# Optimization experiments

Measured on AMD Instinct MI355X. Metric: run time of the kernel, lower is better.

Reference implementation:

```python
import jax, jax.numpy as jnp
import numpy as np

EPS = 1e-8


def setup_inputs() -> dict:
    key = jax.random.key(0)
    k1, k2, k3, k4 = jax.random.split(key, 4)
    b, cin, cout, H, W, ksz = 8, 512, 512, 64, 64, 3
    return {
        "x": jax.random.normal(k1, (b, cin, H, W), dtype=jnp.float32),
        "style": jax.random.normal(k2, (b, cin), dtype=jnp.float32),
        "noise": jax.random.normal(k3, (b, 1, H, W), dtype=jnp.float32),
        "weight": jax.random.normal(k4, (cout, cin, ksz, ksz), dtype=jnp.float32),
        "bias": jnp.zeros((1, cout, 1, 1), dtype=jnp.float32),
        "noise_strength": jnp.zeros((), dtype=jnp.float32),
    }


def reference(x, style, noise, weight, bias, noise_strength):
    cout, cin, k, _ = weight.shape
    b, _, H, W = x.shape
    scale = (1.0 / (cin * k * k)) ** 0.5

    # weight scaled and normalized by per-filter inf-norm
    w = weight * scale / jnp.max(jnp.abs(weight), axis=(1, 2, 3), keepdims=True)
    # style normalized by per-sample inf-norm
    s = style / jnp.max(jnp.abs(style), axis=1, keepdims=True)

    # modulate: (b, cout, cin, k, k)
    w = w[None] * s[:, None, :, None, None]
    # demodulate
    demod = jnp.sqrt(jnp.sum(w * w, axis=(2, 3, 4)) + EPS)  # (b, cout)
    w = w / demod[:, :, None, None, None]

    # grouped conv: one group per sample (note: input is scaled again, as in source)
    xr = (x * scale).reshape(1, b * cin, H, W)
    wr = w.reshape(b * cout, cin, k, k)
    out = jax.lax.conv_general_dilated(
        xr, wr, window_strides=(1, 1), padding=((1, 1), (1, 1)),
        dimension_numbers=("NCHW", "OIHW", "NCHW"), feature_group_count=b)
    out = out.reshape(b, cout, H, W) + bias
    out = out + noise * noise_strength
    return out
```

## Files before the change

kernel.cpp:

```cpp
#include <hip/hip_runtime.h>


#define EPSV   1e-8f
#define SCALEV 0.014731391274719738f

typedef __attribute__((ext_vector_type(8))) short short8;
typedef __attribute__((ext_vector_type(4))) float floatx4;

__device__ __forceinline__ void gload_lds16(const void* g, void* l) {
    __builtin_amdgcn_global_load_lds(
        (const __attribute__((address_space(1))) void*)g,
        (__attribute__((address_space(3))) void*)l, 16, 0, 0);
}

__device__ __forceinline__ unsigned short f2bf(float f) {
    unsigned u = __float_as_uint(f);
    unsigned r = (u + 0x7fffu + ((u >> 16) & 1u)) >> 16;
    return (unsigned short)r;
}

__global__ __launch_bounds__(256) void zero_ws(uint4* __restrict__ p, int n4) {
    uint4 z = {0u, 0u, 0u, 0u};
    int stride = gridDim.x * 256;
    for (int i = blockIdx.x * 256 + threadIdx.x; i < n4; i += stride) p[i] = z;
}

__global__ __launch_bounds__(512) void prep_style(
    const float* __restrict__ style, float* __restrict__ tbuf)
{
    const int b = blockIdx.x, t = threadIdx.x;
    float v = style[b * 512 + t];
    __shared__ float red[512];
    red[t] = fabsf(v);
    __syncthreads();
    for (int s = 256; s > 0; s >>= 1) {
        if (t < s) red[t] = fmaxf(red[t], red[t + s]);
        __syncthreads();
    }
    tbuf[b * 512 + t] = v / red[0];
}

__global__ __launch_bounds__(256) void prep_w(
    const float* __restrict__ weight, float* __restrict__ wsqn,
    unsigned short* __restrict__ Aw)
{
    const int co = blockIdx.x, t = threadIdx.x;
    const float* wp = weight + (size_t)co * 4608;
    float m = 0.f;
    for (int i = t; i < 4608; i += 256) m = fmaxf(m, fabsf(wp[i]));
    __shared__ float red[256];
    red[t] = m;
    __syncthreads();
    for (int s = 128; s > 0; s >>= 1) {
        if (t < s) red[t] = fmaxf(red[t], red[t + s]);
        __syncthreads();
    }
    const float inv = 1.f / red[0];
    for (int ci = t; ci < 512; ci += 256) {
        float s = 0.f;
        #pragma unroll
        for (int k = 0; k < 9; ++k) {
            float v = wp[ci * 9 + k] * inv;
            s = fmaf(v, v, s);
            Aw[(size_t)(co * 9 + k) * 512 + ci] = f2bf(v);
        }
        wsqn[co * 512 + ci] = s;
    }
}

__global__ __launch_bounds__(256) void prep_x(
    const float* __restrict__ x, const float* __restrict__ tbuf,
    unsigned short* __restrict__ xbp)
{
    const int cic = blockIdx.x;
    const int h   = blockIdx.y;
    const int b   = blockIdx.z;
    const int tid = threadIdx.x;
    __shared__ float tr[64][33];

    const int cl = tid >> 3;
    const int w0 = (tid & 7) << 3;
    const int ci = cic * 32 + cl;
    const float tv = tbuf[b * 512 + ci];
    const float* xp = x + (((size_t)(b * 512 + ci)) << 12) + (h << 6) + w0;
    float4 u = *(const float4*)xp;
    float4 v = *(const float4*)(xp + 4);
    tr[w0 + 0][cl] = u.x * tv; tr[w0 + 1][cl] = u.y * tv;
    tr[w0 + 2][cl] = u.z * tv; tr[w0 + 3][cl] = u.w * tv;
    tr[w0 + 4][cl] = v.x * tv; tr[w0 + 5][cl] = v.y * tv;
    tr[w0 + 6][cl] = v.z * tv; tr[w0 + 7][cl] = v.w * tv;
    __syncthreads();

    const int w  = tid >> 2;
    const int c8 = (tid & 3) << 3;
    unsigned short o[8] __attribute__((aligned(16)));
    #pragma unroll
    for (int j = 0; j < 8; ++j) o[j] = f2bf(tr[w][c8 + j]);
    size_t dst = ((size_t)((b * 66 + h + 1) * 66) + (w + 1)) * 512 + cic * 32 + c8;
    *(uint4*)&xbp[dst] = *(const uint4*)o;
}

__global__ __launch_bounds__(256) void gcoef(
    const float* __restrict__ wsqn, const float* __restrict__ tbuf,
    float* __restrict__ gbuf)
{
    const int b    = blockIdx.y;
    const int co   = blockIdx.x * 4 + (threadIdx.x >> 6);
    const int lane = threadIdx.x & 63;
    float sum = 0.f;
    for (int ci = lane; ci < 512; ci += 64) {
        float tv = tbuf[b * 512 + ci];
        sum = fmaf(tv * tv, wsqn[co * 512 + ci], sum);
    }
    #pragma unroll
    for (int off = 32; off > 0; off >>= 1) sum += __shfl_down(sum, off);
    if (lane == 0)
        gbuf[b * 512 + co] = SCALEV * SCALEV / sqrtf(fmaf(SCALEV * SCALEV, sum, EPSV));
}

__global__ __launch_bounds__(256, 2) void conv_mfma(
    const unsigned short* __restrict__ xbp, const unsigned short* __restrict__ Aw,
    const float* __restrict__ gbuf, const float* __restrict__ bias,
    const float* __restrict__ noise, const float* __restrict__ nstr,
    float* __restrict__ out)
{
    __shared__ __align__(16) short sA[2][4096];
    __shared__ __align__(16) short sB[2][6656];

    const int tid  = threadIdx.x;
    const int lane = tid & 63;
    const int wv   = tid >> 6;
    const int b    = blockIdx.z;
    const int co0  = blockIdx.y << 7;
    const int h0   = (blockIdx.x >> 1) << 2;
    const int w0   = (blockIdx.x & 1) << 5;

    const int n0  = lane & 15;
    const int kq  = lane >> 4;
    const int wco = (wv >> 1) << 6;
    const int wpx = (wv & 1) << 6;

    int prow[4], pcol[4], aoff[4];
    #pragma unroll
    for (int fj = 0; fj < 4; ++fj) {
        int p = wpx + fj * 16 + n0;
        prow[fj] = p >> 5;
        pcol[fj] = p & 31;
    }
    #pragma unroll
    for (int fi = 0; fi < 4; ++fi) aoff[fi] = (wco + fi * 16 + n0) * 32 + kq * 8;

    const int sl_px = lane >> 2;
    const int sl_ci = (lane & 3) << 3;

    floatx4 zz = {0.f, 0.f, 0.f, 0.f};
    floatx4 acc[4][4];
    #pragma unroll
    for (int i = 0; i < 4; ++i)
        #pragma unroll
        for (int j = 0; j < 4; ++j) acc[i][j] = zz;

    const unsigned short* xb = xbp + (size_t)b * 4356 * 512;

    for (int ci0 = 0; ci0 < 512; ci0 += 64) {
        __syncthreads();
        #pragma unroll
        for (int hf = 0; hf < 2; ++hf) {
            const unsigned short* src = xb + ci0 + hf * 32 + sl_ci;
            for (int j = wv; j < 13; j += 4) {
                int px = j * 16 + sl_px;
                if (px > 203) px = 203;
                int row = px / 34;
                int col = px - row * 34;
                gload_lds16(src + (((size_t)(h0 + row) * 66 + w0 + col) << 9),
                            &sB[hf][j * 512]);
            }
        }
        #pragma unroll 1
        for (int pos = 0; pos < 9; ++pos) {
            const int kh = pos / 3;
            const int kw = pos - kh * 3;
            if (pos) __syncthreads();
            #pragma unroll
            for (int hf = 0; hf < 2; ++hf) {
                for (int j = wv; j < 8; j += 4) {
                    int co = j * 16 + sl_px;
                    gload_lds16(Aw + (size_t)((co0 + co) * 9 + pos) * 512
                                   + ci0 + hf * 32 + sl_ci,
                                &sA[hf][j * 512]);
                }
            }
            __syncthreads();
            #pragma unroll
            for (int hf = 0; hf < 2; ++hf) {
                short8 af[4], bfr[4];
                #pragma unroll
                for (int fi = 0; fi < 4; ++fi)
                    af[fi] = *(const short8*)&sA[hf][aoff[fi]];
                #pragma unroll
                for (int fj = 0; fj < 4; ++fj)
                    bfr[fj] = *(const short8*)
                        &sB[hf][((prow[fj] + kh) * 34 + pcol[fj] + kw) * 32 + kq * 8];
                #pragma unroll
                for (int fi = 0; fi < 4; ++fi)
                    #pragma unroll
                    for (int fj = 0; fj < 4; ++fj)
                        acc[fi][fj] = __builtin_amdgcn_mfma_f32_16x16x32_bf16(
                            af[fi], bfr[fj], acc[fi][fj], 0, 0, 0);
            }
        }
    }

    const float ns = nstr[0];
    float nz[4];
    int ph[4], pw[4];
    #pragma unroll
    for (int fj = 0; fj < 4; ++fj) {
        int p = wpx + fj * 16 + n0;
        ph[fj] = h0 + (p >> 5);
        pw[fj] = w0 + (p & 31);
        nz[fj] = noise[(b << 12) + (ph[fj] << 6) + pw[fj]] * ns;
    }
    #pragma unroll
    for (int fi = 0; fi < 4; ++fi) {
        #pragma unroll
        for (int i = 0; i < 4; ++i) {
            int co = co0 + wco + fi * 16 + kq * 4 + i;
            float gg = gbuf[(b << 9) + co];
            float bb = bias[co];
            #pragma unroll
            for (int fj = 0; fj < 4; ++fj) {
                out[(((size_t)((b << 9) + co)) << 12) + (ph[fj] << 6) + pw[fj]] =
                    fmaf(gg, acc[fi][fj][i], bb + nz[fj]);
            }
        }
    }
}

extern "C" void kernel_launch(void* const* d_in, const int* in_sizes, int n_in,
                              void* d_out, int out_size, void* d_ws, size_t ws_size,
                              hipStream_t stream)
{
    const float* x      = (const float*)d_in[0];
    const float* style  = (const float*)d_in[1];
    const float* noise  = (const float*)d_in[2];
    const float* weight = (const float*)d_in[3];
    const float* bias   = (const float*)d_in[4];
    const float* nstr   = (const float*)d_in[5];
    float* out = (float*)d_out;
    char* ws = (char*)d_ws;

    float*          tbuf = (float*)(ws);
    float*          gbuf = (float*)(ws + 16384);
    float*          wsqn = (float*)(ws + 32768);
    unsigned short* Aw   = (unsigned short*)(ws + 1081344);
    unsigned short* xbp  = (unsigned short*)(ws + 5799936);

    hipLaunchKernelGGL(zero_ws, dim3(2048), dim3(256), 0, stream,
                       (uint4*)xbp, 35684352 / 16);
    hipLaunchKernelGGL(prep_style, dim3(8), dim3(512), 0, stream, style, tbuf);
    hipLaunchKernelGGL(prep_w, dim3(512), dim3(256), 0, stream, weight, wsqn, Aw);
    hipLaunchKernelGGL(prep_x, dim3(16, 64, 8), dim3(256), 0, stream, x, tbuf, xbp);
    hipLaunchKernelGGL(gcoef, dim3(128, 8), dim3(256), 0, stream, wsqn, tbuf, gbuf);
    hipLaunchKernelGGL(conv_mfma, dim3(32, 4, 8), dim3(256), 0, stream,
                       xbp, Aw, gbuf, bias, noise, nstr, out);
}
```

Baseline: 316.7 us.

## Enlarge conv tile to 256 channels, register-prefetch weights, fuse prep kernels

```diff
diff --git a/kernel.cpp b/kernel.cpp
--- a/kernel.cpp
+++ b/kernel.cpp
@@ -19,12 +19,6 @@
     return (unsigned short)r;
 }
 
-__global__ __launch_bounds__(256) void zero_ws(uint4* __restrict__ p, int n4) {
-    uint4 z = {0u, 0u, 0u, 0u};
-    int stride = gridDim.x * 256;
-    for (int i = blockIdx.x * 256 + threadIdx.x; i < n4; i += stride) p[i] = z;
-}
-
 __global__ __launch_bounds__(512) void prep_style(
     const float* __restrict__ style, float* __restrict__ tbuf)
 {
@@ -41,8 +35,8 @@
 }
 
 __global__ __launch_bounds__(256) void prep_w(
-    const float* __restrict__ weight, float* __restrict__ wsqn,
-    unsigned short* __restrict__ Aw)
+    const float* __restrict__ weight, const float* __restrict__ tbuf,
+    unsigned short* __restrict__ Aw, float* __restrict__ gbuf)
 {
     const int co = blockIdx.x, t = threadIdx.x;
     const float* wp = weight + (size_t)co * 4608;
@@ -56,16 +50,38 @@
         __syncthreads();
     }
     const float inv = 1.f / red[0];
-    for (int ci = t; ci < 512; ci += 256) {
+
+    float sq[2];
+    #pragma unroll
+    for (int j = 0; j < 2; ++j) {
+        int ci = t + j * 256;
         float s = 0.f;
         #pragma unroll
         for (int k = 0; k < 9; ++k) {
             float v = wp[ci * 9 + k] * inv;
             s = fmaf(v, v, s);
-            Aw[(size_t)(co * 9 + k) * 512 + ci] = f2bf(v);
-        }
-        wsqn[co * 512 + ci] = s;
-    }
+            Aw[(size_t)(k * 16 + (ci >> 5)) * 16384 + co * 32 + (ci & 31)] = f2bf(v);
+        }
+        sq[j] = s;
+    }
+
+    __shared__ float red8[8][256];
+    #pragma unroll
+    for (int bb = 0; bb < 8; ++bb) {
+        float t0 = tbuf[bb * 512 + t], t1 = tbuf[bb * 512 + t + 256];
+        red8[bb][t] = t0 * t0 * sq[0] + t1 * t1 * sq[1];
+    }
+    __syncthreads();
+    for (int s = 128; s > 0; s >>= 1) {
+        if (t < s) {
+            #pragma unroll
+            for (int bb = 0; bb < 8; ++bb) red8[bb][t] += red8[bb][t + s];
+        }
+        __syncthreads();
+    }
+    if (t < 8)
+        gbuf[t * 512 + co] =
+            SCALEV * SCALEV / sqrtf(fmaf(SCALEV * SCALEV, red8[t][0], EPSV));
 }
 
 __global__ __launch_bounds__(256) void prep_x(
@@ -96,26 +112,19 @@
     unsigned short o[8] __attribute__((aligned(16)));
     #pragma unroll
     for (int j = 0; j < 8; ++j) o[j] = f2bf(tr[w][c8 + j]);
-    size_t dst = ((size_t)((b * 66 + h + 1) * 66) + (w + 1)) * 512 + cic * 32 + c8;
-    *(uint4*)&xbp[dst] = *(const uint4*)o;
-}
-
-__global__ __launch_bounds__(256) void gcoef(
-    const float* __restrict__ wsqn, const float* __restrict__ tbuf,
-    float* __restrict__ gbuf)
-{
-    const int b    = blockIdx.y;
-    const int co   = blockIdx.x * 4 + (threadIdx.x >> 6);
-    const int lane = threadIdx.x & 63;
-    float sum = 0.f;
-    for (int ci = lane; ci < 512; ci += 64) {
-        float tv = tbuf[b * 512 + ci];
-        sum = fmaf(tv * tv, wsqn[co * 512 + ci], sum);
-    }
-    #pragma unroll
-    for (int off = 32; off > 0; off >>= 1) sum += __shfl_down(sum, off);
-    if (lane == 0)
-        gbuf[b * 512 + co] = SCALEV * SCALEV / sqrtf(fmaf(SCALEV * SCALEV, sum, EPSV));
+    const size_t rowbase = ((size_t)(b * 66 + h + 1)) * 66 * 512 + cic * 32;
+    *(uint4*)&xbp[rowbase + (size_t)(w + 1) * 512 + c8] = *(const uint4*)o;
+
+    uint4 z = {0u, 0u, 0u, 0u};
+    if (tid < 8) {
+        int colsel = (tid >> 2) ? 65 : 0;
+        *(uint4*)&xbp[rowbase + (size_t)colsel * 512 + ((tid & 3) << 3)] = z;
+    }
+    if (h == 0 || h == 63) {
+        const size_t rb = ((size_t)(b * 66) + (h ? 65 : 0)) * 66 * 512 + cic * 32;
+        for (int i = tid; i < 264; i += 256)
+            *(uint4*)&xbp[rb + (size_t)(i >> 2) * 512 + ((i & 3) << 3)] = z;
+    }
 }
 
 __global__ __launch_bounds__(256, 2) void conv_mfma(
@@ -124,91 +133,103 @@
     const float* __restrict__ noise, const float* __restrict__ nstr,
     float* __restrict__ out)
 {
-    __shared__ __align__(16) short sA[2][4096];
-    __shared__ __align__(16) short sB[2][6656];
+    __shared__ __align__(16) short sA[16384];
+    __shared__ __align__(16) short sB[13312];
 
     const int tid  = threadIdx.x;
     const int lane = tid & 63;
     const int wv   = tid >> 6;
     const int b    = blockIdx.z;
-    const int co0  = blockIdx.y << 7;
+    const int co0  = blockIdx.y << 8;
     const int h0   = (blockIdx.x >> 1) << 2;
     const int w0   = (blockIdx.x & 1) << 5;
 
     const int n0  = lane & 15;
     const int kq  = lane >> 4;
-    const int wco = (wv >> 1) << 6;
+    const int wco = (wv >> 1) << 7;
     const int wpx = (wv & 1) << 6;
 
-    int prow[4], pcol[4], aoff[4];
+    int prow[4], pcol[4];
     #pragma unroll
     for (int fj = 0; fj < 4; ++fj) {
         int p = wpx + fj * 16 + n0;
         prow[fj] = p >> 5;
         pcol[fj] = p & 31;
     }
-    #pragma unroll
-    for (int fi = 0; fi < 4; ++fi) aoff[fi] = (wco + fi * 16 + n0) * 32 + kq * 8;
+    int aoff[8];
+    #pragma unroll
+    for (int fi = 0; fi < 8; ++fi) aoff[fi] = (wco + fi * 16 + n0) * 32 + kq * 8;
 
     const int sl_px = lane >> 2;
     const int sl_ci = (lane & 3) << 3;
 
     floatx4 zz = {0.f, 0.f, 0.f, 0.f};
-    floatx4 acc[4][4];
-    #pragma unroll
-    for (int i = 0; i < 4; ++i)
+    floatx4 acc[8][4];
+    #pragma unroll
+    for (int i = 0; i < 8; ++i)
         #pragma unroll
         for (int j = 0; j < 4; ++j) acc[i][j] = zz;
 
-    const unsigned short* xb = xbp + (size_t)b * 4356 * 512;
-
-    for (int ci0 = 0; ci0 < 512; ci0 += 64) {
-        __syncthreads();
-        #pragma unroll
-        for (int hf = 0; hf < 2; ++hf) {
-            const unsigned short* src = xb + ci0 + hf * 32 + sl_ci;
-            for (int j = wv; j < 13; j += 4) {
-                int px = j * 16 + sl_px;
-                if (px > 203) px = 203;
-                int row = px / 34;
-                int col = px - row * 34;
-                gload_lds16(src + (((size_t)(h0 + row) * 66 + w0 + col) << 9),
-                            &sB[hf][j * 512]);
-            }
-        }
-        #pragma unroll 1
-        for (int pos = 0; pos < 9; ++pos) {
-            const int kh = pos / 3;
-            const int kw = pos - kh * 3;
-            if (pos) __syncthreads();
+    const unsigned short* xb = xbp + (size_t)b * (4356 * 512);
+    const unsigned short* awb = Aw + (co0 << 5);
+
+    uint4 pf[8];
+    #pragma unroll
+    for (int c = 0; c < 8; ++c) {
+        int s = c * 2048 + tid * 8;
+        pf[c] = *(const uint4*)&awb[(size_t)(s >> 13) * 16384 + (s & 8191)];
+    }
+
+    int pos = 0, cislab = 0;
+    #pragma unroll 1
+    for (int it = 0; it < 72; ++it) {
+        __syncthreads();
+        #pragma unroll
+        for (int c = 0; c < 8; ++c)
+            *(uint4*)&sA[c * 2048 + tid * 8] = pf[c];
+        if (pos == 0) {
             #pragma unroll
             for (int hf = 0; hf < 2; ++hf) {
-                for (int j = wv; j < 8; j += 4) {
-                    int co = j * 16 + sl_px;
-                    gload_lds16(Aw + (size_t)((co0 + co) * 9 + pos) * 512
-                                   + ci0 + hf * 32 + sl_ci,
-                                &sA[hf][j * 512]);
+                const unsigned short* src = xb + ((cislab + hf) << 5) + sl_ci;
+                for (int j = wv; j < 13; j += 4) {
+                    int px = j * 16 + sl_px;
+                    if (px > 203) px = 203;
+                    int row = px / 34, col = px - row * 34;
+                    gload_lds16(src + (((size_t)(h0 + row) * 66 + w0 + col) << 9),
+                                &sB[hf * 6656 + j * 512]);
                 }
             }
-            __syncthreads();
-            #pragma unroll
-            for (int hf = 0; hf < 2; ++hf) {
-                short8 af[4], bfr[4];
-                #pragma unroll
-                for (int fi = 0; fi < 4; ++fi)
-                    af[fi] = *(const short8*)&sA[hf][aoff[fi]];
+        }
+        __syncthreads();
+        if (it < 71) {
+            int pn = pos + 1, cn = cislab;
+            if (pn == 9) { pn = 0; cn += 2; }
+            #pragma unroll
+            for (int c = 0; c < 8; ++c) {
+                int s = c * 2048 + tid * 8;
+                pf[c] = *(const uint4*)
+                    &awb[(size_t)(pn * 16 + cn + (s >> 13)) * 16384 + (s & 8191)];
+            }
+        }
+        const int kh = pos / 3, kw = pos - kh * 3;
+        #pragma unroll
+        for (int hf = 0; hf < 2; ++hf) {
+            short8 af[8], bfr[4];
+            #pragma unroll
+            for (int fi = 0; fi < 8; ++fi)
+                af[fi] = *(const short8*)&sA[hf * 8192 + aoff[fi]];
+            #pragma unroll
+            for (int fj = 0; fj < 4; ++fj)
+                bfr[fj] = *(const short8*)
+                    &sB[hf * 6656 + ((prow[fj] + kh) * 34 + pcol[fj] + kw) * 32 + kq * 8];
+            #pragma unroll
+            for (int fi = 0; fi < 8; ++fi)
                 #pragma unroll
                 for (int fj = 0; fj < 4; ++fj)
-                    bfr[fj] = *(const short8*)
-                        &sB[hf][((prow[fj] + kh) * 34 + pcol[fj] + kw) * 32 + kq * 8];
-                #pragma unroll
-                for (int fi = 0; fi < 4; ++fi)
-                    #pragma unroll
-                    for (int fj = 0; fj < 4; ++fj)
-                        acc[fi][fj] = __builtin_amdgcn_mfma_f32_16x16x32_bf16(
-                            af[fi], bfr[fj], acc[fi][fj], 0, 0, 0);
-            }
-        }
+                    acc[fi][fj] = __builtin_amdgcn_mfma_f32_16x16x32_bf16(
+                        af[fi], bfr[fj], acc[fi][fj], 0, 0, 0);
+        }
+        if (++pos == 9) { pos = 0; cislab += 2; }
     }
 
     const float ns = nstr[0];
@@ -222,7 +243,7 @@
         nz[fj] = noise[(b << 12) + (ph[fj] << 6) + pw[fj]] * ns;
     }
     #pragma unroll
-    for (int fi = 0; fi < 4; ++fi) {
+    for (int fi = 0; fi < 8; ++fi) {
         #pragma unroll
         for (int i = 0; i < 4; ++i) {
             int co = co0 + wco + fi * 16 + kq * 4 + i;
@@ -252,16 +273,12 @@
 
     float*          tbuf = (float*)(ws);
     float*          gbuf = (float*)(ws + 16384);
-    float*          wsqn = (float*)(ws + 32768);
-    unsigned short* Aw   = (unsigned short*)(ws + 1081344);
-    unsigned short* xbp  = (unsigned short*)(ws + 5799936);
-
-    hipLaunchKernelGGL(zero_ws, dim3(2048), dim3(256), 0, stream,
-                       (uint4*)xbp, 35684352 / 16);
+    unsigned short* Aw   = (unsigned short*)(ws + 32768);
+    unsigned short* xbp  = (unsigned short*)(ws + 4751360);
+
     hipLaunchKernelGGL(prep_style, dim3(8), dim3(512), 0, stream, style, tbuf);
-    hipLaunchKernelGGL(prep_w, dim3(512), dim3(256), 0, stream, weight, wsqn, Aw);
+    hipLaunchKernelGGL(prep_w, dim3(512), dim3(256), 0, stream, weight, tbuf, Aw, gbuf);
     hipLaunchKernelGGL(prep_x, dim3(16, 64, 8), dim3(256), 0, stream, x, tbuf, xbp);
-    hipLaunchKernelGGL(gcoef, dim3(128, 8), dim3(256), 0, stream, wsqn, tbuf, gbuf);
-    hipLaunchKernelGGL(conv_mfma, dim3(32, 4, 8), dim3(256), 0, stream,
+    hipLaunchKernelGGL(conv_mfma, dim3(32, 2, 8), dim3(256), 0, stream,
                        xbp, Aw, gbuf, bias, noise, nstr, out);
 }
```

New measurement: 480.3 us. 1.52x slower.
